# Kernel optimization log

Measured on AMD Instinct MI355X. Metric: run time of the kernel, lower is better.

The kernel has to match this reference:

```python
import jax, jax.numpy as jnp
import numpy as np

H, DK, D, DFF = 8, 64, 512, 512
B, S = 4, 1024
SCALE = 1.0 / np.sqrt(DK)


def _ln(x, g, b, eps=1e-5):
    m = jnp.mean(x, axis=-1, keepdims=True)
    v = jnp.mean((x - m) ** 2, axis=-1, keepdims=True)
    return (x - m) / jnp.sqrt(v + eps) * g + b


def _heads(x, w, b):
    bs, s, _ = x.shape
    return (x @ w + b).reshape(bs, s, H, DK).transpose(0, 2, 1, 3)  # [B,H,S,DK]


def _encoder_layer(x, qw, qb, kw, kb, vw, vb, ow, ob, g1, b1, w1, c1, w2, c2, g2, b2):
    # standard post-LN transformer encoder layer (sub_attention.Encoder(1))
    q = _heads(x, qw, qb)
    k = _heads(x, kw, kb)
    v = _heads(x, vw, vb)
    attn = jax.nn.softmax(jnp.einsum('bhqd,bhkd->bhqk', q, k) * SCALE, axis=-1)
    ctx = jnp.einsum('bhqk,bhkd->bhqd', attn, v).transpose(0, 2, 1, 3).reshape(x.shape[0], -1, H * DK)
    h = _ln(ctx @ ow + ob + x, g1, b1)
    f = jax.nn.relu(h @ w1 + c1) @ w2 + c2
    return _ln(f + h, g2, b2)


def setup_inputs() -> dict:
    key = jax.random.key(0)
    ks = iter(jax.random.split(key, 80))

    def nrm(*shape):
        return jax.random.normal(next(ks), shape, jnp.float32) * 0.02

    inp = {'audio_feat': jax.random.normal(next(ks), (B, S, D), jnp.float32),
           'video_feat': jax.random.normal(next(ks), (B, S, D), jnp.float32)}
    for p in ['aq', 'ak', 'av', 'vq', 'vk', 'vv', 'out']:
        inp[p + '_w'] = nrm(D, D)
        inp[p + '_b'] = jnp.zeros((D,), jnp.float32)
    inp['ln_g'] = jnp.ones((D,), jnp.float32)
    inp['ln_b'] = jnp.zeros((D,), jnp.float32)
    for pfx in ['asa_', 'vsa_']:
        for wn in ['qw', 'kw', 'vw', 'ow']:
            inp[pfx + wn] = nrm(D, D)
        for bn in ['qb', 'kb', 'vb', 'ob']:
            inp[pfx + bn] = jnp.zeros((D,), jnp.float32)
        inp[pfx + 'w1'] = nrm(D, DFF)
        inp[pfx + 'c1'] = jnp.zeros((DFF,), jnp.float32)
        inp[pfx + 'w2'] = nrm(DFF, D)
        inp[pfx + 'c2'] = jnp.zeros((D,), jnp.float32)
        inp[pfx + 'g1'] = jnp.ones((D,), jnp.float32)
        inp[pfx + 'b1'] = jnp.zeros((D,), jnp.float32)
        inp[pfx + 'g2'] = jnp.ones((D,), jnp.float32)
        inp[pfx + 'b2'] = jnp.zeros((D,), jnp.float32)
    return inp


def reference(audio_feat, video_feat, aq_w, aq_b, ak_w, ak_b, av_w, av_b, vq_w, vq_b, vk_w, vk_b, vv_w, vv_b, out_w, out_b, ln_g, ln_b, asa_qw, asa_qb, asa_kw, asa_kb, asa_vw, asa_vb, asa_ow, asa_ob, asa_g1, asa_b1, asa_w1, asa_c1, asa_w2, asa_c2, asa_g2, asa_b2, vsa_qw, vsa_qb, vsa_kw, vsa_kb, vsa_vw, vsa_vb, vsa_ow, vsa_ob, vsa_g1, vsa_b1, vsa_w1, vsa_c1, vsa_w2, vsa_c2, vsa_g2, vsa_b2):
    audio_self = _encoder_layer(audio_feat, asa_qw, asa_qb, asa_kw, asa_kb, asa_vw, asa_vb, asa_ow, asa_ob, asa_g1, asa_b1, asa_w1, asa_c1, asa_w2, asa_c2, asa_g2, asa_b2)
    video_self = _encoder_layer(video_feat, vsa_qw, vsa_qb, vsa_kw, vsa_kb, vsa_vw, vsa_vb, vsa_ow, vsa_ob, vsa_g1, vsa_b1, vsa_w1, vsa_c1, vsa_w2, vsa_c2, vsa_g2, vsa_b2)
    qa = _heads(audio_feat, aq_w, aq_b)
    ka = _heads(audio_feat, ak_w, ak_b)
    va = _heads(audio_feat, av_w, av_b)
    qv = _heads(video_feat, vq_w, vq_b)
    kv = _heads(video_feat, vk_w, vk_b)
    vvh = _heads(video_feat, vv_w, vv_b)
    attn_a = jax.nn.softmax(jnp.einsum('bhqd,bhkd->bhqk', qa, ka) * SCALE, axis=-1)
    attn_v = jax.nn.softmax(jnp.einsum('bhqd,bhkd->bhqk', qv, kv) * SCALE, axis=-1)
    attn = attn_a * attn_v  # dual-softmax elementwise combine
    ctx = jnp.einsum('bhqk,bhkd->bhqd', attn, va) * jnp.einsum('bhqk,bhkd->bhqd', attn, vvh)
    ctx = ctx.transpose(0, 2, 1, 3).reshape(audio_feat.shape[0], -1, H * DK)
    context = ctx @ out_w + out_b
    return _ln(audio_feat + context + audio_self + video_self, ln_g, ln_b)
```

## Files before the change

kernel.cpp:

```cpp
#include <hip/hip_runtime.h>
#include <cstddef>
#include <cstdint>


typedef __attribute__((ext_vector_type(8))) short s8v;
typedef __attribute__((ext_vector_type(4))) short s4v;
typedef __attribute__((ext_vector_type(4))) float f4v;

#define QSC 0.1803368801111444f
#define EXP2(x) __builtin_amdgcn_exp2f(x)
#define WAITV(N) asm volatile("s_waitcnt vmcnt(" #N ")" ::: "memory")
#define BAR() __builtin_amdgcn_s_barrier()
#define PRIO(n) __builtin_amdgcn_s_setprio(n)

static __device__ __forceinline__ short f2bf(float f){
  unsigned int u = __builtin_bit_cast(unsigned int, f);
  u += 0x7fffu + ((u >> 16) & 1u);
  return (short)(u >> 16);
}
static __device__ __forceinline__ float bf2f(short s){
  unsigned int u = ((unsigned int)(unsigned short)s) << 16;
  return __builtin_bit_cast(float, u);
}
static __device__ __forceinline__ void gload16(const void* g, void* l){
  __builtin_amdgcn_global_load_lds(
      (const __attribute__((address_space(1))) unsigned int*)g,
      (__attribute__((address_space(3))) unsigned int*)l, 16, 0, 0);
}
#define MFMA16(a,b,c) __builtin_amdgcn_mfma_f32_16x16x32_bf16(a,b,c,0,0,0)

struct Ptr19 { const float* p[19]; };

__global__ __launch_bounds__(256) void prep(const float* __restrict__ a,
                                            const float* __restrict__ v,
                                            short* __restrict__ oa,
                                            short* __restrict__ ov,
                                            Ptr19 ws, short* __restrict__ wp){
  const int b = blockIdx.x, tid = threadIdx.x;
  if (b < 2048){
    const float* src = (b >= 1024) ? v : a;
    short* dst = (b >= 1024) ? ov : oa;
    const int i = ((b & 1023) * 256 + tid) * 8;
    float4 x = *reinterpret_cast<const float4*>(src + i);
    float4 y = *reinterpret_cast<const float4*>(src + i + 4);
    s8v o;
    o[0]=f2bf(x.x); o[1]=f2bf(x.y); o[2]=f2bf(x.z); o[3]=f2bf(x.w);
    o[4]=f2bf(y.x); o[5]=f2bf(y.y); o[6]=f2bf(y.z); o[7]=f2bf(y.w);
    *reinterpret_cast<s8v*>(dst + i) = o;
  } else {
    const int pb = b - 2048;
    const int mat = pb >> 7;
    const float* W = ws.p[mat];
    const int f = (pb & 127) * 256 + tid;
    const int nblk = f >> 10, kg = (f >> 4) & 63, nl = f & 15;
    const int n = nblk * 16 + nl, k = kg * 8;
    s8v o;
#pragma unroll
    for (int e = 0; e < 8; ++e) o[e] = f2bf(W[(size_t)(k + e) * 512 + n]);
    *reinterpret_cast<s8v*>(wp + (size_t)mat * 262144 + (size_t)f * 8) = o;
  }
}

struct GemmJobs { const short* A[12]; const short* W[12]; const float* bias[12];
                  short* C[12]; int mode[12]; };

__global__ __launch_bounds__(256, 2) void gemm_wide(GemmJobs J){
  int i = (blockIdx.z * 32 + blockIdx.y) * 2 + blockIdx.x;
  const int c = (64 * gridDim.z) >> 3;
  i = (i & 7) * c + (i >> 3);
  const int z = i >> 6, rem = i & 63;
  const int by = rem >> 1, bx = rem & 1;

  const short* __restrict__ A = J.A[z];
  const short* __restrict__ Wp = J.W[z];
  const float* __restrict__ bias = J.bias[z];
  short* __restrict__ C = J.C[z];
  const int md = J.mode[z];
  __shared__ short smem[36864];
  const int tid = threadIdx.x, lane = tid & 63, w = tid >> 6;
  const int wm = w >> 1, wn = w & 1;
  const int m0 = by * 128, n0 = bx * 256;
  const int lh = lane >> 4, ll = lane & 15;
  f4v acc[4][8] = {};

  auto stage = [&](int kt, int buf){
    const int k0 = kt * 32;
    short* As = smem + buf * 4096;
    short* Bs = smem + 12288 + buf * 8192;
#pragma unroll
    for (int p = 0; p < 2; ++p){
      const int f = tid + 256 * p;
      const int blk = f >> 6, kg = (f >> 4) & 3, il = f & 15;
      gload16(A + (size_t)(m0 + blk * 16 + il) * 512 + k0 + kg * 8, As + f * 8);
    }
#pragma unroll
    for (int p = 0; p < 4; ++p){
      const int f = tid + 256 * p;
      const int cblk = f >> 6, kg = (f >> 4) & 3, il = f & 15;
      gload16(Wp + ((size_t)(((n0 >> 4) + cblk) * 64 + (k0 >> 3) + kg) * 16 + il) * 8,
              Bs + f * 8);
    }
  };

  stage(0, 0);
  stage(1, 1);
#pragma unroll 1
  for (int kt = 0; kt < 16; ++kt){
    if (kt < 15) { WAITV(6); } else { WAITV(0); }
    BAR();
    if (kt < 14) stage(kt + 2, (kt + 2) % 3);
    const int cur = kt % 3;
    const short* As = smem + cur * 4096;
    const short* Bs = smem + 12288 + cur * 8192;
    s8v a[4], b[8];
#pragma unroll
    for (int q = 0; q < 4; ++q)
      a[q] = *reinterpret_cast<const s8v*>(&As[(((wm*4+q)*4 + lh)*16 + ll) * 8]);
#pragma unroll
    for (int j = 0; j < 8; ++j)
      b[j] = *reinterpret_cast<const s8v*>(&Bs[(((wn*8+j)*4 + lh)*16 + ll) * 8]);
    PRIO(1);
#pragma unroll
    for (int q = 0; q < 4; ++q)
#pragma unroll
      for (int j = 0; j < 8; ++j)
        acc[q][j] = MFMA16(a[q], b[j], acc[q][j]);
    PRIO(0);
  }
  BAR();

  if (md == 2){
#pragma unroll
    for (int j = 0; j < 8; ++j){
      const int col = n0 + wn * 128 + j * 16 + ll;
      const float bv = bias[col];
      const int hh = col >> 6, dl = col & 63, dblk = dl >> 4, il = dl & 15;
#pragma unroll
      for (int q = 0; q < 4; ++q){
        const int rowb = m0 + wm * 64 + q * 16 + lh * 4;
        const int bb = rowb >> 10, srow = rowb & 1023;
        const size_t off = ((size_t)((bb*8 + hh)*16 + (srow >> 6))) * 4096
                         + (size_t)(((dblk << 7) + (((srow >> 3) & 7) << 4) + il) * 8 + (srow & 7));
        s4v o4;
#pragma unroll
        for (int r = 0; r < 4; ++r) o4[r] = f2bf(acc[q][j][r] + bv);
        *reinterpret_cast<s4v*>(&C[off]) = o4;
      }
    }
  } else {
    short* epi = smem + w * 8192;
    const float sc = (md == 1) ? QSC : 1.0f;
#pragma unroll
    for (int j = 0; j < 8; ++j){
      const float bv = bias[n0 + wn * 128 + j * 16 + ll];
#pragma unroll
      for (int q = 0; q < 4; ++q)
#pragma unroll
        for (int r = 0; r < 4; ++r)
          epi[(q*16 + lh*4 + r)*128 + j*16 + ll] = f2bf((acc[q][j][r] + bv) * sc);
    }
#pragma unroll
    for (int i2 = 0; i2 < 16; ++i2){
      const int row = i2 * 4 + (lane >> 4);
      s8v vr = *reinterpret_cast<const s8v*>(&epi[row*128 + (lane & 15)*8]);
      *reinterpret_cast<s8v*>(&C[(size_t)(m0 + wm*64 + row)*512 + n0 + wn*128 + (lane&15)*8]) = vr;
    }
  }
}

template<bool RELU>
__global__ __launch_bounds__(256) void gemm_n64(GemmJobs J){
  int i = (blockIdx.z * 32 + blockIdx.y) * 8 + blockIdx.x;
  const int c = (256 * gridDim.z) >> 3;
  i = (i & 7) * c + (i >> 3);
  const int z = i >> 8, rem = i & 255;
  const int by = rem >> 3, bx = rem & 7;

  const short* __restrict__ A = J.A[z];
  const short* __restrict__ Wp = J.W[z];
  const float* __restrict__ bias = J.bias[z];
  short* __restrict__ C = J.C[z];
  __shared__ short As[3][4096], Bs[3][2048];
  const int tid = threadIdx.x, lane = tid & 63, w = tid >> 6;
  const int wm = w >> 1, wn = w & 1;
  const int m0 = by * 128, n0 = bx * 64;
  const int lh = lane >> 4, ll = lane & 15;
  f4v acc[4][2] = {};

  auto stage = [&](int kt, int buf){
    const int k0 = kt * 32;
#pragma unroll
    for (int p = 0; p < 2; ++p){
      const int f = tid + 256 * p;
      const int blk = f >> 6, kg = (f >> 4) & 3, il = f & 15;
      gload16(A + (size_t)(m0 + blk * 16 + il) * 512 + k0 + kg * 8, &As[buf][f * 8]);
    }
    {
      const int f = tid;
      const int blk = f >> 6, kg = (f >> 4) & 3, il = f & 15;
      gload16(Wp + ((size_t)(((n0 >> 4) + blk) * 64 + (k0 >> 3) + kg) * 16 + il) * 8,
              &Bs[buf][f * 8]);
    }
  };

  stage(0, 0);
  stage(1, 1);
#pragma unroll 1
  for (int kt = 0; kt < 16; ++kt){
    if (kt < 15) { WAITV(3); } else { WAITV(0); }
    BAR();
    if (kt < 14) stage(kt + 2, (kt + 2) % 3);
    const int cur = kt % 3;
    s8v a[4], b[2];
#pragma unroll
    for (int q = 0; q < 4; ++q)
      a[q] = *reinterpret_cast<const s8v*>(&As[cur][(((wm*4+q)*4 + lh)*16 + ll) * 8]);
#pragma unroll
    for (int j = 0; j < 2; ++j)
      b[j] = *reinterpret_cast<const s8v*>(&Bs[cur][(((wn*2+j)*4 + lh)*16 + ll) * 8]);
    PRIO(1);
#pragma unroll
    for (int q = 0; q < 4; ++q)
#pragma unroll
      for (int j = 0; j < 2; ++j)
        acc[q][j] = MFMA16(a[q], b[j], acc[q][j]);
    PRIO(0);
  }
  BAR();

  short* epi = &As[0][0] + w * 2048;
#pragma unroll
  for (int j = 0; j < 2; ++j){
    const float bv = bias[n0 + wn * 32 + j * 16 + ll];
#pragma unroll
    for (int q = 0; q < 4; ++q)
#pragma unroll
      for (int r = 0; r < 4; ++r){
        float v = acc[q][j][r] + bv;
        if (RELU) v = fmaxf(v, 0.f);
        epi[(q*16 + lh*4 + r)*32 + j*16 + ll] = f2bf(v);
      }
  }
#pragma unroll
  for (int i2 = 0; i2 < 4; ++i2){
    const int row = i2 * 16 + (lane >> 2);
    s8v vr = *reinterpret_cast<const s8v*>(&epi[row*32 + (lane & 3)*8]);
    *reinterpret_cast<s8v*>(&C[(size_t)(m0 + wm*64 + row)*512 + n0 + wn*32 + (lane&3)*8]) = vr;
  }
}

struct AttnJob { const short* Q; const short* K; const short* Vp; short* O; };

__global__ __launch_bounds__(512) void attn_enc(AttnJob j0, AttnJob j1){
  const AttnJob jb = blockIdx.z ? j1 : j0;
  __shared__ short KT[2][4096], VT[2][4096];
  __shared__ short PL[8][1024];
  const int tid = threadIdx.x, lane = tid & 63, w = tid >> 6;
  int bi = blockIdx.y * 8 + blockIdx.x;
  bi = (bi & 7) * 32 + (bi >> 3);
  const int qt = bi & 7, bh = bi >> 3;
  const int b = bh >> 3, h = bh & 7;
  const int q0 = qt * 128;
  const size_t base = (size_t)b * 1024 * 512 + (size_t)h * 64;
  const int lh = lane >> 4, ll = lane & 15;
  short* PLw = PL[w];

  s8v qf[2];
#pragma unroll
  for (int df = 0; df < 2; ++df)
    qf[df] = *reinterpret_cast<const s8v*>(jb.Q + base + (size_t)(q0 + w*16 + ll)*512 + lh*8 + df*32);

  const int sblk = tid >> 7, sg8 = (tid >> 4) & 7, sil = tid & 15;
  auto stage = [&](int it, int buf){
    gload16(jb.K + base + (size_t)(it*64 + sblk*16 + sil)*512 + sg8*8, &KT[buf][tid*8]);
    gload16(jb.Vp + ((size_t)bh*16 + it)*4096 + (size_t)tid*8, &VT[buf][tid*8]);
  };

  f4v o[4] = {};
  float zacc = 0.f;
  const int pwo = ((lh >> 1) * 16 + ll) * 8 + (lh & 1) * 4;
  const int pro = ((lh) * 16 + ll) * 8;

  stage(0, 0);
#pragma unroll 1
  for (int it = 0; it < 16; ++it){
    if (it < 15) { stage(it + 1, (it + 1) & 1); WAITV(2); }
    else         { WAITV(0); }
    BAR();
    const int cur = it & 1;

    f4v s[4] = {};
    PRIO(1);
#pragma unroll
    for (int fn = 0; fn < 4; ++fn)
#pragma unroll
      for (int df = 0; df < 2; ++df){
        s8v kf = *reinterpret_cast<const s8v*>(&KT[cur][((fn*8 + lh + df*4)*16 + ll) * 8]);
        s[fn] = MFMA16(kf, qf[df], s[fn]);
      }
    PRIO(0);

#pragma unroll
    for (int fn = 0; fn < 4; ++fn){
      s4v p4;
#pragma unroll
      for (int r = 0; r < 4; ++r){
        const float p = EXP2(s[fn][r]);
        zacc += p;
        p4[r] = f2bf(p);
      }
      *reinterpret_cast<s4v*>(&PLw[fn*256 + pwo]) = p4;
    }
    s8v pa[2];
#pragma unroll
    for (int kf2 = 0; kf2 < 2; ++kf2)
      pa[kf2] = *reinterpret_cast<const s8v*>(&PLw[kf2*512 + pro]);
    PRIO(1);
#pragma unroll
    for (int fd = 0; fd < 4; ++fd)
#pragma unroll
      for (int kf2 = 0; kf2 < 2; ++kf2){
        s8v vf = *reinterpret_cast<const s8v*>(&VT[cur][((fd*8 + lh + kf2*4)*16 + ll) * 8]);
        o[fd] = MFMA16(vf, pa[kf2], o[fd]);
      }
    PRIO(0);
    BAR();
  }

  float Z = zacc;
  Z += __shfl_xor(Z, 16); Z += __shfl_xor(Z, 32);
  const float rz = 1.f / Z;
#pragma unroll
  for (int fd = 0; fd < 4; ++fd){
    s4v o4;
#pragma unroll
    for (int r = 0; r < 4; ++r) o4[r] = f2bf(o[fd][r] * rz);
    *reinterpret_cast<s4v*>(&jb.O[base + (size_t)(q0 + w*16 + ll)*512 + fd*16 + lh*4]) = o4;
  }
}

__global__ __launch_bounds__(512) void attn_dual(const short* __restrict__ Qa, const short* __restrict__ Ka,
                                                 const short* __restrict__ Vap, const short* __restrict__ Qv,
                                                 const short* __restrict__ Kv, const short* __restrict__ Vvp,
                                                 short* __restrict__ O){
  __shared__ short KTa[2][4096], KTv[2][4096], VTa[2][4096], VTv[2][4096];
  __shared__ short PL[8][1024];
  const int tid = threadIdx.x, lane = tid & 63, w = tid >> 6;
  int bi = blockIdx.y * 8 + blockIdx.x;
  bi = (bi & 7) * 32 + (bi >> 3);
  const int qt = bi & 7, bh = bi >> 3;
  const int b = bh >> 3, h = bh & 7;
  const int q0 = qt * 128;
  const size_t base = (size_t)b * 1024 * 512 + (size_t)h * 64;
  const int lh = lane >> 4, ll = lane & 15;
  short* PLw = PL[w];

  s8v qfa[2], qfv[2];
#pragma unroll
  for (int df = 0; df < 2; ++df){
    const size_t ro = base + (size_t)(q0 + w*16 + ll)*512 + lh*8 + df*32;
    qfa[df] = *reinterpret_cast<const s8v*>(Qa + ro);
    qfv[df] = *reinterpret_cast<const s8v*>(Qv + ro);
  }

  const int sblk = tid >> 7, sg8 = (tid >> 4) & 7, sil = tid & 15;
  auto stage = [&](int it, int buf){
    const size_t krow = base + (size_t)(it*64 + sblk*16 + sil)*512 + sg8*8;
    gload16(Ka + krow, &KTa[buf][tid*8]);
    gload16(Kv + krow, &KTv[buf][tid*8]);
    const size_t voff = ((size_t)bh*16 + it)*4096 + (size_t)tid*8;
    gload16(Vap + voff, &VTa[buf][tid*8]);
    gload16(Vvp + voff, &VTv[buf][tid*8]);
  };

  f4v oa[4] = {}, ov[4] = {};
  float za = 0.f, zv = 0.f;
  const int pwo = ((lh >> 1) * 16 + ll) * 8 + (lh & 1) * 4;
  const int pro = ((lh) * 16 + ll) * 8;

  stage(0, 0);
#pragma unroll 1
  for (int it = 0; it < 16; ++it){
    if (it < 15) { stage(it + 1, (it + 1) & 1); WAITV(4); }
    else         { WAITV(0); }
    BAR();
    const int cur = it & 1;

    f4v sa[4] = {}, sv[4] = {};
    PRIO(1);
#pragma unroll
    for (int fn = 0; fn < 4; ++fn)
#pragma unroll
      for (int df = 0; df < 2; ++df){
        const int boff = ((fn*8 + lh + df*4)*16 + ll) * 8;
        s8v ka = *reinterpret_cast<const s8v*>(&KTa[cur][boff]);
        s8v kv = *reinterpret_cast<const s8v*>(&KTv[cur][boff]);
        sa[fn] = MFMA16(ka, qfa[df], sa[fn]);
        sv[fn] = MFMA16(kv, qfv[df], sv[fn]);
      }
    PRIO(0);

#pragma unroll
    for (int fn = 0; fn < 4; ++fn){
      s4v p4;
#pragma unroll
      for (int r = 0; r < 4; ++r){
        const float ea = EXP2(sa[fn][r]);
        const float ev = EXP2(sv[fn][r]);
        za += ea; zv += ev;
        p4[r] = f2bf(ea * ev);
      }
      *reinterpret_cast<s4v*>(&PLw[fn*256 + pwo]) = p4;
    }
    s8v pa[2];
#pragma unroll
    for (int kf2 = 0; kf2 < 2; ++kf2)
      pa[kf2] = *reinterpret_cast<const s8v*>(&PLw[kf2*512 + pro]);
    PRIO(1);
#pragma unroll
    for (int fd = 0; fd < 4; ++fd)
#pragma unroll
      for (int kf2 = 0; kf2 < 2; ++kf2){
        const int boff = ((fd*8 + lh + kf2*4)*16 + ll) * 8;
        s8v va = *reinterpret_cast<const s8v*>(&VTa[cur][boff]);
        s8v vv = *reinterpret_cast<const s8v*>(&VTv[cur][boff]);
        oa[fd] = MFMA16(va, pa[kf2], oa[fd]);
        ov[fd] = MFMA16(vv, pa[kf2], ov[fd]);
      }
    PRIO(0);
    BAR();
  }

  float Za = za, Zv = zv;
  Za += __shfl_xor(Za, 16); Za += __shfl_xor(Za, 32);
  Zv += __shfl_xor(Zv, 16); Zv += __shfl_xor(Zv, 32);
  const float rz = 1.f / (Za * Zv);
#pragma unroll
  for (int fd = 0; fd < 4; ++fd){
    s4v o4;
#pragma unroll
    for (int r = 0; r < 4; ++r){
      const float v = (oa[fd][r] * rz) * (ov[fd][r] * rz);
      o4[r] = f2bf(v);
    }
    *reinterpret_cast<s4v*>(&O[base + (size_t)(q0 + w*16 + ll)*512 + fd*16 + lh*4]) = o4;
  }
}

struct LnJob { const short* xb0; const short* xb1; const short* xb2;
               const float* xf; const float* g; const float* bb; void* out; };

template<int NBF, bool ADDF32, bool OUTF32>
__global__ __launch_bounds__(256) void ln_fused(LnJob j0, LnJob j1){
  const LnJob j = blockIdx.y ? j1 : j0;
  const int row = blockIdx.x, t = threadIdx.x;
  const size_t base = (size_t)row * 512;
  float x[2];
#pragma unroll
  for (int u = 0; u < 2; ++u){
    const int c = t + u * 256;
    float v = bf2f(j.xb0[base + c]);
    if (NBF > 1) v += bf2f(j.xb1[base + c]);
    if (NBF > 2) v += bf2f(j.xb2[base + c]);
    if (ADDF32) v += j.xf[base + c];
    x[u] = v;
  }
  float s = x[0] + x[1], ss = x[0]*x[0] + x[1]*x[1];
#pragma unroll
  for (int o = 32; o; o >>= 1){ s += __shfl_xor(s, o); ss += __shfl_xor(ss, o); }
  __shared__ float rb[8];
  const int wv = t >> 6;
  if ((t & 63) == 0){ rb[wv] = s; rb[wv + 4] = ss; }
  __syncthreads();
  s  = rb[0] + rb[1] + rb[2] + rb[3];
  ss = rb[4] + rb[5] + rb[6] + rb[7];
  const float m = s * (1.f / 512.f);
  const float var = ss * (1.f / 512.f) - m * m;
  const float rstd = rsqrtf(var + 1e-5f);
#pragma unroll
  for (int u = 0; u < 2; ++u){
    const int c = t + u * 256;
    const float v = (x[u] - m) * rstd * j.g[c] + j.bb[c];
    if (OUTF32) ((float*)j.out)[base + c] = v;
    else        ((short*)j.out)[base + c] = f2bf(v);
  }
}

__global__ __launch_bounds__(256) void ln_final(const short* __restrict__ fa, const short* __restrict__ ha,
                                                const short* __restrict__ fv, const short* __restrict__ hv,
                                                const short* __restrict__ ctx, const float* __restrict__ audio,
                                                const float* __restrict__ g2a, const float* __restrict__ b2a,
                                                const float* __restrict__ g2v, const float* __restrict__ b2v,
                                                const float* __restrict__ gf, const float* __restrict__ bf,
                                                float* __restrict__ out){
  const int row = blockIdx.x, t = threadIdx.x;
  const size_t base = (size_t)row * 512;
  __shared__ float rb[24];
  const int wv = t >> 6;

  auto reduce2 = [&](float a, float b, int p){
    float s = a + b, ss = a*a + b*b;
#pragma unroll
    for (int o = 32; o; o >>= 1){ s += __shfl_xor(s, o); ss += __shfl_xor(ss, o); }
    if ((t & 63) == 0){ rb[p*8 + wv] = s; rb[p*8 + 4 + wv] = ss; }
  };
  auto stats = [&](int p, float& m, float& rstd){
    const float s  = rb[p*8+0] + rb[p*8+1] + rb[p*8+2] + rb[p*8+3];
    const float ss = rb[p*8+4] + rb[p*8+5] + rb[p*8+6] + rb[p*8+7];
    m = s * (1.f / 512.f);
    rstd = rsqrtf(ss * (1.f / 512.f) - m * m + 1e-5f);
  };

  float xa[2], xv[2];
#pragma unroll
  for (int u = 0; u < 2; ++u){
    const int c = t + u * 256;
    xa[u] = bf2f(fa[base + c]) + bf2f(ha[base + c]);
    xv[u] = bf2f(fv[base + c]) + bf2f(hv[base + c]);
  }
  reduce2(xa[0], xa[1], 0);
  reduce2(xv[0], xv[1], 1);
  __syncthreads();
  float ma, ra, mv, rv;
  stats(0, ma, ra);
  stats(1, mv, rv);

  float xf[2];
#pragma unroll
  for (int u = 0; u < 2; ++u){
    const int c = t + u * 256;
    const float sa = (xa[u] - ma) * ra * g2a[c] + b2a[c];
    const float sv = (xv[u] - mv) * rv * g2v[c] + b2v[c];
    xf[u] = audio[base + c] + bf2f(ctx[base + c]) + sa + sv;
  }
  reduce2(xf[0], xf[1], 2);
  __syncthreads();
  float mf, rf;
  stats(2, mf, rf);
#pragma unroll
  for (int u = 0; u < 2; ++u){
    const int c = t + u * 256;
    out[base + c] = (xf[u] - mf) * rf * gf[c] + bf[c];
  }
}

extern "C" void kernel_launch(void* const* d_in, const int* in_sizes, int n_in,
                              void* d_out, int out_size, void* d_ws, size_t ws_size,
                              hipStream_t stream) {
  const float* audio = (const float*)d_in[0];
  const float* video = (const float*)d_in[1];
  auto F = [&](int i){ return (const float*)d_in[i]; };

  short* ws16 = (short*)d_ws;
  const size_t SL = 2097152;
  auto S = [&](int i){ return ws16 + (size_t)i * SL; };
  short* Wp = S(12);
  auto WP = [&](int i){ return (const short*)(Wp + (size_t)i * 262144); };
  short* Kcv = (short*)d_out;
  short* Vcv = (short*)d_out + SL;

  Ptr19 pw;
  const int widx[19] = {18,19,20,21,26,28, 34,35,36,37,42,44, 2,4,6,8,10,12, 14};
  for (int i = 0; i < 19; ++i) pw.p[i] = F(widx[i]);
  prep<<<4480, 256, 0, stream>>>(audio, video, S(10), S(11), pw, Wp);

  GemmJobs g1{};
  const short* g1A[12] = {S(10),S(10),S(10), S(11),S(11),S(11), S(10),S(10),S(10), S(11),S(11),S(11)};
  const short* g1W[12] = {WP(0),WP(1),WP(2), WP(6),WP(7),WP(8), WP(12),WP(13),WP(14), WP(15),WP(16),WP(17)};
  const float* g1B[12] = {F(22),F(23),F(24), F(38),F(39),F(40), F(3),F(5),F(7), F(9),F(11),F(13)};
  short*       g1C[12] = {S(0),S(1),S(2), S(3),S(4),S(5), S(6),S(7),S(8), S(9),Kcv,Vcv};
  const int    g1M[12] = {1,0,2, 1,0,2, 1,0,2, 1,0,2};
  for (int i = 0; i < 12; ++i){ g1.A[i]=g1A[i]; g1.W[i]=g1W[i]; g1.bias[i]=g1B[i]; g1.C[i]=g1C[i]; g1.mode[i]=g1M[i]; }
  gemm_wide<<<dim3(2,32,12), 256, 0, stream>>>(g1);

  attn_enc<<<dim3(8,32,2), 512, 0, stream>>>(AttnJob{S(0),S(1),S(2),S(10)},
                                             AttnJob{S(3),S(4),S(5),S(11)});

  attn_dual<<<dim3(8,32), 512, 0, stream>>>(S(6),S(7),S(8), S(9),Kcv,Vcv, S(0));

  GemmJobs g39{};
  g39.A[0]=S(10); g39.W[0]=WP(3);  g39.bias[0]=F(25); g39.C[0]=S(1); g39.mode[0]=0;
  g39.A[1]=S(11); g39.W[1]=WP(9);  g39.bias[1]=F(41); g39.C[1]=S(2); g39.mode[1]=0;
  g39.A[2]=S(0);  g39.W[2]=WP(18); g39.bias[2]=F(15); g39.C[2]=S(3); g39.mode[2]=0;
  gemm_n64<false><<<dim3(8,32,3), 256, 0, stream>>>(g39);

  ln_fused<1,true,false><<<dim3(4096,2), 256, 0, stream>>>(
      LnJob{S(1),nullptr,nullptr, audio, F(30),F(31), S(4)},
      LnJob{S(2),nullptr,nullptr, video, F(46),F(47), S(5)});

  GemmJobs g5{};
  g5.A[0]=S(4); g5.W[0]=WP(4);  g5.bias[0]=F(27); g5.C[0]=S(6); g5.mode[0]=0;
  g5.A[1]=S(5); g5.W[1]=WP(10); g5.bias[1]=F(43); g5.C[1]=S(7); g5.mode[1]=0;
  gemm_n64<true><<<dim3(8,32,2), 256, 0, stream>>>(g5);

  GemmJobs g6{};
  g6.A[0]=S(6); g6.W[0]=WP(5);  g6.bias[0]=F(29); g6.C[0]=S(8); g6.mode[0]=0;
  g6.A[1]=S(7); g6.W[1]=WP(11); g6.bias[1]=F(45); g6.C[1]=S(9); g6.mode[1]=0;
  gemm_n64<false><<<dim3(8,32,2), 256, 0, stream>>>(g6);

  ln_final<<<4096, 256, 0, stream>>>(S(8),S(4), S(9),S(5), S(3), audio,
                                     F(32),F(33), F(48),F(49), F(16),F(17),
                                     (float*)d_out);
}
```

Measured before the change: 177.4 us.

## Split dual-attention key range across two wave groups with 64-row query tiles

```diff
diff --git a/kernel.cpp b/kernel.cpp
--- a/kernel.cpp
+++ b/kernel.cpp
@@ -343,40 +343,47 @@
                                                  const short* __restrict__ Vap, const short* __restrict__ Qv,
                                                  const short* __restrict__ Kv, const short* __restrict__ Vvp,
                                                  short* __restrict__ O){
-  __shared__ short KTa[2][4096], KTv[2][4096], VTa[2][4096], VTv[2][4096];
-  __shared__ short PL[8][1024];
+  __shared__ short smem[36864];
   const int tid = threadIdx.x, lane = tid & 63, w = tid >> 6;
-  int bi = blockIdx.y * 8 + blockIdx.x;
-  bi = (bi & 7) * 32 + (bi >> 3);
-  const int qt = bi & 7, bh = bi >> 3;
+  const int qw = w & 3, kh = w >> 2;
+  int bi = blockIdx.y * 16 + blockIdx.x;
+  bi = (bi & 7) * 64 + (bi >> 3);
+  const int qt = bi & 15, bh = bi >> 4;
   const int b = bh >> 3, h = bh & 7;
-  const int q0 = qt * 128;
+  const int q0 = qt * 64;
   const size_t base = (size_t)b * 1024 * 512 + (size_t)h * 64;
   const int lh = lane >> 4, ll = lane & 15;
-  short* PLw = PL[w];
+  short* PLw = smem + 32768 + w * 512;
 
   s8v qfa[2], qfv[2];
 #pragma unroll
   for (int df = 0; df < 2; ++df){
-    const size_t ro = base + (size_t)(q0 + w*16 + ll)*512 + lh*8 + df*32;
+    const size_t ro = base + (size_t)(q0 + qw*16 + ll)*512 + lh*8 + df*32;
     qfa[df] = *reinterpret_cast<const s8v*>(Qa + ro);
     qfv[df] = *reinterpret_cast<const s8v*>(Qv + ro);
   }
 
-  const int sblk = tid >> 7, sg8 = (tid >> 4) & 7, sil = tid & 15;
+  const int hh = tid >> 8;
+  const int u = tid & 255;
+  const int kblk = u >> 7, kg8 = (u >> 4) & 7, kil = u & 15;
+  const int vdb = u >> 6, vk4 = (u >> 4) & 3,  vil = u & 15;
+
   auto stage = [&](int it, int buf){
-    const size_t krow = base + (size_t)(it*64 + sblk*16 + sil)*512 + sg8*8;
-    gload16(Ka + krow, &KTa[buf][tid*8]);
-    gload16(Kv + krow, &KTv[buf][tid*8]);
-    const size_t voff = ((size_t)bh*16 + it)*4096 + (size_t)tid*8;
-    gload16(Vap + voff, &VTa[buf][tid*8]);
-    gload16(Vvp + voff, &VTv[buf][tid*8]);
+    const int dso = hh * 4096 + buf * 2048 + u * 8;
+    const size_t krow = base + (size_t)(hh*512 + it*32 + kblk*16 + kil)*512 + kg8*8;
+    gload16(Ka + krow, smem + dso);
+    gload16(Kv + krow, smem + 8192 + dso);
+    const int kt16 = hh*8 + (it >> 1);
+    const int kgrp = (it & 1)*4 + vk4;
+    const size_t voff = ((size_t)bh*16 + kt16)*4096 + (size_t)((vdb*8 + kgrp)*16 + vil)*8;
+    gload16(Vap + voff, smem + 16384 + dso);
+    gload16(Vvp + voff, smem + 24576 + dso);
   };
 
   f4v oa[4] = {}, ov[4] = {};
   float za = 0.f, zv = 0.f;
   const int pwo = ((lh >> 1) * 16 + ll) * 8 + (lh & 1) * 4;
-  const int pro = ((lh) * 16 + ll) * 8;
+  const int pro = (lh * 16 + ll) * 8;
 
   stage(0, 0);
 #pragma unroll 1
@@ -385,23 +392,28 @@
     else         { WAITV(0); }
     BAR();
     const int cur = it & 1;
-
-    f4v sa[4] = {}, sv[4] = {};
+    const int to = kh * 4096 + cur * 2048;
+    const short* pKa = smem + to;
+    const short* pKv = smem + 8192 + to;
+    const short* pVa = smem + 16384 + to;
+    const short* pVv = smem + 24576 + to;
+
+    f4v sa[2] = {}, sv[2] = {};
     PRIO(1);
 #pragma unroll
-    for (int fn = 0; fn < 4; ++fn)
+    for (int fn = 0; fn < 2; ++fn)
 #pragma unroll
       for (int df = 0; df < 2; ++df){
-        const int boff = ((fn*8 + lh + df*4)*16 + ll) * 8;
-        s8v ka = *reinterpret_cast<const s8v*>(&KTa[cur][boff]);
-        s8v kv = *reinterpret_cast<const s8v*>(&KTv[cur][boff]);
+        const int boff = (fn*128 + (lh + df*4)*16 + ll) * 8;
+        s8v ka = *reinterpret_cast<const s8v*>(&pKa[boff]);
+        s8v kv = *reinterpret_cast<const s8v*>(&pKv[boff]);
         sa[fn] = MFMA16(ka, qfa[df], sa[fn]);
         sv[fn] = MFMA16(kv, qfv[df], sv[fn]);
       }
     PRIO(0);
 
 #pragma unroll
-    for (int fn = 0; fn < 4; ++fn){
+    for (int fn = 0; fn < 2; ++fn){
       s4v p4;
 #pragma unroll
       for (int r = 0; r < 4; ++r){
@@ -412,38 +424,57 @@
       }
       *reinterpret_cast<s4v*>(&PLw[fn*256 + pwo]) = p4;
     }
-    s8v pa[2];
-#pragma unroll
-    for (int kf2 = 0; kf2 < 2; ++kf2)
-      pa[kf2] = *reinterpret_cast<const s8v*>(&PLw[kf2*512 + pro]);
+    s8v pa = *reinterpret_cast<const s8v*>(&PLw[pro]);
     PRIO(1);
 #pragma unroll
-    for (int fd = 0; fd < 4; ++fd)
-#pragma unroll
-      for (int kf2 = 0; kf2 < 2; ++kf2){
-        const int boff = ((fd*8 + lh + kf2*4)*16 + ll) * 8;
-        s8v va = *reinterpret_cast<const s8v*>(&VTa[cur][boff]);
-        s8v vv = *reinterpret_cast<const s8v*>(&VTv[cur][boff]);
-        oa[fd] = MFMA16(va, pa[kf2], oa[fd]);
-        ov[fd] = MFMA16(vv, pa[kf2], ov[fd]);
-      }
+    for (int fd = 0; fd < 4; ++fd){
+      const int voff2 = (fd*64 + lh*16 + ll) * 8;
+      s8v va = *reinterpret_cast<const s8v*>(&pVa[voff2]);
+      s8v vv = *reinterpret_cast<const s8v*>(&pVv[voff2]);
+      oa[fd] = MFMA16(va, pa, oa[fd]);
+      ov[fd] = MFMA16(vv, pa, ov[fd]);
+    }
     PRIO(0);
     BAR();
   }
 
-  float Za = za, Zv = zv;
-  Za += __shfl_xor(Za, 16); Za += __shfl_xor(Za, 32);
-  Zv += __shfl_xor(Zv, 16); Zv += __shfl_xor(Zv, 32);
-  const float rz = 1.f / (Za * Zv);
-#pragma unroll
-  for (int fd = 0; fd < 4; ++fd){
-    s4v o4;
-#pragma unroll
-    for (int r = 0; r < 4; ++r){
-      const float v = (oa[fd][r] * rz) * (ov[fd][r] * rz);
-      o4[r] = f2bf(v);
-    }
-    *reinterpret_cast<s4v*>(&O[base + (size_t)(q0 + w*16 + ll)*512 + fd*16 + lh*4]) = o4;
+  float* cb = (float*)smem;
+  const int idx = qw * 64 + lane;
+  if (kh == 1){
+#pragma unroll
+    for (int fd = 0; fd < 4; ++fd)
+#pragma unroll
+      for (int r = 0; r < 4; ++r){
+        cb[(fd*4 + r)*256 + idx] = oa[fd][r];
+        cb[(16 + fd*4 + r)*256 + idx] = ov[fd][r];
+      }
+    cb[32*256 + idx] = za;
+    cb[33*256 + idx] = zv;
+  }
+  BAR();
+  if (kh == 0){
+#pragma unroll
+    for (int fd = 0; fd < 4; ++fd)
+#pragma unroll
+      for (int r = 0; r < 4; ++r){
+        oa[fd][r] += cb[(fd*4 + r)*256 + idx];
+        ov[fd][r] += cb[(16 + fd*4 + r)*256 + idx];
+      }
+    float Za = za + cb[32*256 + idx];
+    float Zv = zv + cb[33*256 + idx];
+    Za += __shfl_xor(Za, 16); Za += __shfl_xor(Za, 32);
+    Zv += __shfl_xor(Zv, 16); Zv += __shfl_xor(Zv, 32);
+    const float rz = 1.f / (Za * Zv);
+#pragma unroll
+    for (int fd = 0; fd < 4; ++fd){
+      s4v o4;
+#pragma unroll
+      for (int r = 0; r < 4; ++r){
+        const float v = (oa[fd][r] * rz) * (ov[fd][r] * rz);
+        o4[r] = f2bf(v);
+      }
+      *reinterpret_cast<s4v*>(&O[base + (size_t)(q0 + qw*16 + ll)*512 + fd*16 + lh*4]) = o4;
+    }
   }
 }
 
@@ -576,7 +607,7 @@
   attn_enc<<<dim3(8,32,2), 512, 0, stream>>>(AttnJob{S(0),S(1),S(2),S(10)},
                                              AttnJob{S(3),S(4),S(5),S(11)});
 
-  attn_dual<<<dim3(8,32), 512, 0, stream>>>(S(6),S(7),S(8), S(9),Kcv,Vcv, S(0));
+  attn_dual<<<dim3(16,32), 512, 0, stream>>>(S(6),S(7),S(8), S(9),Kcv,Vcv, S(0));
 
   GemmJobs g39{};
   g39.A[0]=S(10); g39.W[0]=WP(3);  g39.bias[0]=F(25); g39.C[0]=S(1); g39.mode[0]=0;
```

After: 173.7 us (median of 2 runs). 1.02x faster.
